# Performance work log

Measured on AMD Instinct MI355X. Metric: run time of the kernel, lower is better.

Reference implementation:

```python
import jax, jax.numpy as jnp
import numpy as np

VOCAB, EMBED, HIDDEN = 32000, 512, 1024
B, T = 2, 2048
LN_EPS = 1e-5


def setup_inputs() -> dict:
    key = jax.random.key(0)
    ks = jax.random.split(key, 12)

    def xavier(k, fan_in, fan_out):
        lim = float(np.sqrt(6.0 / (fan_in + fan_out)))
        return jax.random.uniform(k, (fan_in, fan_out), jnp.float32, -lim, lim)

    return {
        "tokens": jax.random.randint(ks[0], (B, T), 0, VOCAB),
        "E": xavier(ks[1], VOCAB, EMBED),                    # embedding table
        "Wc": xavier(ks[2], EMBED, HIDDEN),                  # fc_current (stored [in,out])
        "bc": jnp.full((HIDDEN,), 0.01, jnp.float32),
        "Wh": xavier(ks[3], EMBED, HIDDEN),                  # fc_context
        "bh": jnp.full((HIDDEN,), 0.01, jnp.float32),
        "Wm": xavier(ks[4], 2 * HIDDEN, HIDDEN),             # fc_merge
        "bm": jnp.full((HIDDEN,), 0.01, jnp.float32),
        "Wo": xavier(ks[5], HIDDEN, VOCAB),                  # fc_out
        "bo": jnp.full((VOCAB,), 0.01, jnp.float32),
        "ln_w": jnp.ones((HIDDEN,), jnp.float32),
        "ln_b": jnp.zeros((HIDDEN,), jnp.float32),
    }


def reference(tokens, E, Wc, bc, Wh, bh, Wm, bm, Wo, bo, ln_w, ln_b):
    emb = E[tokens]  # [B, T, D]
    # history mean at step t = mean(emb[:, :t]); at t==0 the module uses current embed
    csum = jnp.cumsum(emb, axis=1)
    counts = jnp.arange(1, T, dtype=emb.dtype)[None, :, None]
    hist_mean = jnp.concatenate([emb[:, :1], csum[:, :-1] / counts], axis=1)  # [B,T,D]

    cur_enc = jax.nn.relu(jnp.einsum("btd,dh->bth", emb, Wc) + bc)
    hist_enc = jax.nn.relu(jnp.einsum("btd,dh->bth", hist_mean, Wh) + bh)
    merged = jnp.concatenate([cur_enc, hist_enc], axis=-1)  # [B,T,2H]
    merged = jax.nn.relu(jnp.einsum("btk,kh->bth", merged, Wm) + bm)

    mu = jnp.mean(merged, axis=-1, keepdims=True)
    var = jnp.mean(jnp.square(merged - mu), axis=-1, keepdims=True)
    normed = (merged - mu) * jax.lax.rsqrt(var + LN_EPS) * ln_w + ln_b

    logits = (jnp.einsum("bth,hv->btv", normed, Wo) + bo) / 10.0  # [B,T,V]
    return logits
```

## Files before the change

### kernel.cpp

```cpp
#include <hip/hip_runtime.h>
#include <hip/hip_bf16.h>
#include <stdint.h>
#include <stdio.h>

#define T_SEQ  2048
#define BATCH  2
#define NROWS  4096
#define EMBED  512
#define HIDDEN 1024
#define VOCAB  32000
#define NCHUNK 32
#define CHLEN  64

typedef __bf16 bf16x8 __attribute__((ext_vector_type(8)));
typedef float  f32x4  __attribute__((ext_vector_type(4)));

__device__ __forceinline__ float b2f(unsigned short h) {
  union { unsigned int u; float f; } v; v.u = ((unsigned int)h) << 16; return v.f;
}
__device__ __forceinline__ unsigned short f2b(float f) {
  union { float f; unsigned int u; } v; v.f = f;
  unsigned int u = v.u;
  u += 0x7fffu + ((u >> 16) & 1u);
  return (unsigned short)(u >> 16);
}

__global__ void gather_kernel(const int* __restrict__ tokens,
                              const float* __restrict__ E,
                              unsigned short* __restrict__ emb) {
  const int row = blockIdx.x;
  const int tok = tokens[row];
  const float2 v = ((const float2*)(E + (size_t)tok * EMBED))[threadIdx.x];
  const uint32_t packed = (uint32_t)f2b(v.x) | ((uint32_t)f2b(v.y) << 16);
  ((uint32_t*)(emb + (size_t)row * EMBED))[threadIdx.x] = packed;
}

__global__ void scan_sum_kernel(const unsigned short* __restrict__ emb,
                                float* __restrict__ csum) {
  const int bc = blockIdx.x;
  const int d  = threadIdx.x;
  const unsigned short* e = emb + ((size_t)bc * CHLEN) * EMBED + d;
  float s = 0.f;
  #pragma unroll 8
  for (int i = 0; i < CHLEN; ++i) s += b2f(e[(size_t)i * EMBED]);
  csum[(size_t)bc * EMBED + d] = s;
}

__global__ void scan_excl_kernel(float* __restrict__ csum) {
  const int b = blockIdx.x;
  const int d = threadIdx.x;
  float run = 0.f;
  for (int c = 0; c < NCHUNK; ++c) {
    const size_t idx = ((size_t)b * NCHUNK + c) * EMBED + d;
    const float v = csum[idx];
    csum[idx] = run;
    run += v;
  }
}

__global__ void scan_emit_kernel(const unsigned short* __restrict__ emb,
                                 const float* __restrict__ csum,
                                 unsigned short* __restrict__ hist) {
  const int bc = blockIdx.x;
  const int c  = bc & (NCHUNK - 1);
  const int d  = threadIdx.x;
  const unsigned short* e = emb  + ((size_t)bc * CHLEN) * EMBED + d;
  unsigned short*       h = hist + ((size_t)bc * CHLEN) * EMBED + d;
  float sum = csum[(size_t)bc * EMBED + d];
  #pragma unroll 8
  for (int i = 0; i < CHLEN; ++i) {
    const int t = c * CHLEN + i;
    h[(size_t)i * EMBED] = (t == 0) ? e[0] : f2b(sum / (float)t);
    sum += b2f(e[(size_t)i * EMBED]);
  }
}

__global__ void transpose_cast_kernel(const float* __restrict__ in,
                                      unsigned short* __restrict__ out,
                                      int R, int C) {
  __shared__ float tile[32][33];
  const int tx = threadIdx.x & 31;
  const int ty = threadIdx.x >> 5;
  const int r0 = blockIdx.y * 32, c0 = blockIdx.x * 32;
  #pragma unroll
  for (int i = 0; i < 32; i += 8)
    tile[ty + i][tx] = in[(size_t)(r0 + ty + i) * C + (c0 + tx)];
  __syncthreads();
  #pragma unroll
  for (int i = 0; i < 32; i += 8)
    out[(size_t)(c0 + ty + i) * R + (r0 + tx)] = f2b(tile[tx][ty + i]);
}

__device__ __forceinline__ void async16(unsigned short* lds, const unsigned short* g) {
  __builtin_amdgcn_global_load_lds(
      (const __attribute__((address_space(1))) void*)g,
      (__attribute__((address_space(3))) void*)lds, 16, 0, 0);
}

#define BM 128
#define BN 128
#define BK 32

template<int MODE>
__global__ __launch_bounds__(256) void gemm_bt_kernel(
    const unsigned short* __restrict__ A,
    const unsigned short* __restrict__ BT,
    const float* __restrict__ bias,
    void* __restrict__ out, int M, int N, int K, int ldOut, int colOff,
    const unsigned short* __restrict__ A2,
    const unsigned short* __restrict__ BT2,
    const float* __restrict__ bias2, int colOff2) {
  __shared__ unsigned short As[BM * BK];
  __shared__ unsigned short Bs[BN * BK];

  const unsigned short* Ap = A;
  const unsigned short* Bp = BT;
  const float*          bp = bias;
  int                   co = colOff;
  if (blockIdx.z) { Ap = A2; Bp = BT2; bp = bias2; co = colOff2; }

  int wg = blockIdx.x;
  {
    const int nwg = gridDim.x;
    const int xcd = wg & 7, loc = wg >> 3;
    const int q = nwg >> 3, r = nwg & 7;
    wg = (xcd < r ? xcd * (q + 1) : r * (q + 1) + (xcd - r) * q) + loc;
  }
  const int nmb = M / BM;
  const int mb  = wg % nmb;
  const int nb  = wg / nmb;
  const int m0  = mb * BM;
  const int n0  = nb * BN;

  const int tid  = threadIdx.x;
  const int wave = tid >> 6;
  const int lane = tid & 63;
  const int wm = (wave & 1) * 64;
  const int wn = (wave >> 1) * 64;

  const int srow = (wave << 5) + (lane >> 2);
  const int scol = (lane & 3) << 3;
  const unsigned short* aSrc = Ap + (size_t)(m0 + srow) * K + scol;
  const unsigned short* bSrc = Bp + (size_t)(n0 + srow) * K + scol;
  unsigned short* aDst = As + (wave << 5) * BK;
  unsigned short* bDst = Bs + (wave << 5) * BK;

  f32x4 acc[4][4];
  #pragma unroll
  for (int i = 0; i < 4; ++i)
    #pragma unroll
    for (int j = 0; j < 4; ++j)
      acc[i][j] = (f32x4){0.f, 0.f, 0.f, 0.f};

  const int q = lane >> 4;
  const int r = lane & 15;

  for (int k0 = 0; k0 < K; k0 += BK) {
    __syncthreads();
    async16(aDst,           aSrc);
    async16(aDst + 16 * BK, aSrc + 16 * (size_t)K);
    async16(bDst,           bSrc);
    async16(bDst + 16 * BK, bSrc + 16 * (size_t)K);
    aSrc += BK; bSrc += BK;
    __syncthreads();

    bf16x8 af[4], bfr[4];
    #pragma unroll
    for (int mi = 0; mi < 4; ++mi)
      af[mi] = *(const bf16x8*)&As[(wm + mi * 16 + r) * BK + (q << 3)];
    #pragma unroll
    for (int ni = 0; ni < 4; ++ni)
      bfr[ni] = *(const bf16x8*)&Bs[(wn + ni * 16 + r) * BK + (q << 3)];
    #pragma unroll
    for (int mi = 0; mi < 4; ++mi)
      #pragma unroll
      for (int ni = 0; ni < 4; ++ni)
        acc[mi][ni] = __builtin_amdgcn_mfma_f32_16x16x32_bf16(
            af[mi], bfr[ni], acc[mi][ni], 0, 0, 0);
  }

  #pragma unroll
  for (int ni = 0; ni < 4; ++ni) {
    const int col = n0 + wn + ni * 16 + r;
    const float bv = bp[col];
    #pragma unroll
    for (int mi = 0; mi < 4; ++mi) {
      #pragma unroll
      for (int e = 0; e < 4; ++e) {
        const int row = m0 + wm + mi * 16 + (q << 2) + e;
        float v = acc[mi][ni][e] + bv;
        if (MODE == 0 || MODE == 1) v = fmaxf(v, 0.f);
        if (MODE == 2) v *= 0.1f;
        const size_t idx = (size_t)row * ldOut + co + col;
        if (MODE == 0) ((unsigned short*)out)[idx] = f2b(v);
        else           ((float*)out)[idx] = v;
      }
    }
  }
}


#define BAR() do {                            \
    asm volatile("" ::: "memory");            \
    __builtin_amdgcn_sched_barrier(0);        \
    __builtin_amdgcn_s_barrier();             \
    __builtin_amdgcn_sched_barrier(0);        \
    asm volatile("" ::: "memory");            \
  } while (0)

__global__ __launch_bounds__(512, 2) void gemm256_out_kernel(
    const unsigned short* __restrict__ A,
    const unsigned short* __restrict__ BT,
    const float* __restrict__ bias,
    float* __restrict__ out, int M, int N, int K, int ldOut) {
  __shared__ unsigned short lds[2][2][2][8192];

  int wg = blockIdx.x;
  {
    const int nwg = gridDim.x;
    const int xcd = wg & 7, loc = wg >> 3;
    const int q8 = nwg >> 3, r8 = nwg & 7;
    wg = (xcd < r8 ? xcd * (q8 + 1) : r8 * (q8 + 1) + (xcd - r8) * q8) + loc;
  }
  const int nmb = M >> 8;
  const int mb = wg % nmb, nb = wg / nmb;
  const int m0 = mb << 8, n0 = nb << 8;

  const int tid  = threadIdx.x;
  const int wave = tid >> 6, lane = tid & 63;
  const int wr = wave >> 2, wc = wave & 3;
  const int q = lane >> 4, r = lane & 15, rr = lane & 7;

  const int srow = (wave << 4) + (lane >> 3);
  const int scol = ((lane & 7) ^ (lane >> 3)) << 3;
  const unsigned short* aB = A  + (size_t)(m0 + srow) * K + scol;
  const unsigned short* bB = BT + (size_t)(n0 + srow) * K + scol;

  const int NTt = K >> 6;

  auto stage = [&](int matB, int h, int tb, int kt) {
    unsigned short* d = &lds[tb][matB][h][wave << 10];
    const unsigned short* s =
        (matB ? bB : aB) + (size_t)h * 128 * K + ((size_t)kt << 6);
    async16(d, s);
    async16(d + 512, s + ((size_t)K << 3));
  };

  auto ldA = [&](int tb, int mi, int ks) {
    return *(const bf16x8*)&lds[tb][0][wr]
        [(mi * 16 + r) * 64 + ((((ks << 2) | q) ^ rr) << 3)];
  };
  auto ldB = [&](int tb, int ni, int ks) {
    return *(const bf16x8*)&lds[tb][1][wc >> 1]
        [(((wc & 1) << 6) + ni * 16 + r) * 64 + ((((ks << 2) | q) ^ rr) << 3)];
  };

  f32x4 acc[8][4];
  #pragma unroll
  for (int i = 0; i < 8; ++i)
    #pragma unroll
    for (int j = 0; j < 4; ++j)
      acc[i][j] = (f32x4){0.f, 0.f, 0.f, 0.f};

  bf16x8 afr[8][2], bfr[2][2];

  stage(0, 0, 0, 0); stage(0, 1, 0, 0); stage(1, 0, 0, 0); stage(1, 1, 0, 0);
  if (NTt > 1) {
    stage(0, 0, 1, 1); stage(0, 1, 1, 1); stage(1, 0, 1, 1);
    asm volatile("s_waitcnt vmcnt(6)" ::: "memory");
  } else {
    asm volatile("s_waitcnt vmcnt(0)" ::: "memory");
  }
  BAR();

#define TILE(U, BU) do {                                                       \
    const int u_ = (U);                                                        \
                            \
    _Pragma("unroll")                                                          \
    for (int mi = 0; mi < 4; ++mi) {                                           \
      afr[mi][0] = ldA(BU, mi, 0); afr[mi][1] = ldA(BU, mi, 1);                \
    }                                                                          \
    _Pragma("unroll")                                                          \
    for (int nj = 0; nj < 2; ++nj) {                                           \
      bfr[nj][0] = ldB(BU, nj, 0); bfr[nj][1] = ldB(BU, nj, 1);                \
    }                                                                          \
    if (u_ + 1 < NTt) stage(1, 1, 1 - (BU), u_ + 1);                           \
    __builtin_amdgcn_s_setprio(1);                                             \
    _Pragma("unroll")                                                          \
    for (int mi = 0; mi < 4; ++mi)                                             \
      _Pragma("unroll")                                                        \
      for (int nj = 0; nj < 2; ++nj) {                                         \
        acc[mi][nj] = __builtin_amdgcn_mfma_f32_16x16x32_bf16(                 \
            afr[mi][0], bfr[nj][0], acc[mi][nj], 0, 0, 0);                     \
        acc[mi][nj] = __builtin_amdgcn_mfma_f32_16x16x32_bf16(                 \
            afr[mi][1], bfr[nj][1], acc[mi][nj], 0, 0, 0);                     \
      }                                                                        \
    __builtin_amdgcn_s_setprio(0);                                             \
    BAR();                                                                     \
                                 \
    _Pragma("unroll")                                                          \
    for (int mi = 4; mi < 8; ++mi) {                                           \
      afr[mi][0] = ldA(BU, mi, 0); afr[mi][1] = ldA(BU, mi, 1);                \
    }                                                                          \
    __builtin_amdgcn_s_setprio(1);                                             \
    _Pragma("unroll")                                                          \
    for (int mi = 4; mi < 8; ++mi)                                             \
      _Pragma("unroll")                                                        \
      for (int nj = 0; nj < 2; ++nj) {                                         \
        acc[mi][nj] = __builtin_amdgcn_mfma_f32_16x16x32_bf16(                 \
            afr[mi][0], bfr[nj][0], acc[mi][nj], 0, 0, 0);                     \
        acc[mi][nj] = __builtin_amdgcn_mfma_f32_16x16x32_bf16(                 \
            afr[mi][1], bfr[nj][1], acc[mi][nj], 0, 0, 0);                     \
      }                                                                        \
    __builtin_amdgcn_s_setprio(0);                                             \
    BAR();                                                                     \
                            \
    _Pragma("unroll")                                                          \
    for (int nj = 0; nj < 2; ++nj) {                                           \
      bfr[nj][0] = ldB(BU, 2 + nj, 0); bfr[nj][1] = ldB(BU, 2 + nj, 1);        \
    }                                                                          \
    if (u_ + 2 < NTt) stage(0, 0, BU, u_ + 2);                                 \
    __builtin_amdgcn_s_setprio(1);                                             \
    _Pragma("unroll")                                                          \
    for (int mi = 0; mi < 4; ++mi)                                             \
      _Pragma("unroll")                                                        \
      for (int nj = 0; nj < 2; ++nj) {                                         \
        acc[mi][2 + nj] = __builtin_amdgcn_mfma_f32_16x16x32_bf16(             \
            afr[mi][0], bfr[nj][0], acc[mi][2 + nj], 0, 0, 0);                 \
        acc[mi][2 + nj] = __builtin_amdgcn_mfma_f32_16x16x32_bf16(             \
            afr[mi][1], bfr[nj][1], acc[mi][2 + nj], 0, 0, 0);                 \
      }                                                                        \
    __builtin_amdgcn_s_setprio(0);                                             \
    BAR();                                                                     \
                   \
    if (u_ + 2 < NTt) { stage(0, 1, BU, u_ + 2); stage(1, 0, BU, u_ + 2); }    \
    __builtin_amdgcn_s_setprio(1);                                             \
    _Pragma("unroll")                                                          \
    for (int mi = 4; mi < 8; ++mi)                                             \
      _Pragma("unroll")                                                        \
      for (int nj = 0; nj < 2; ++nj) {                                         \
        acc[mi][2 + nj] = __builtin_amdgcn_mfma_f32_16x16x32_bf16(             \
            afr[mi][0], bfr[nj][0], acc[mi][2 + nj], 0, 0, 0);                 \
        acc[mi][2 + nj] = __builtin_amdgcn_mfma_f32_16x16x32_bf16(             \
            afr[mi][1], bfr[nj][1], acc[mi][2 + nj], 0, 0, 0);                 \
      }                                                                        \
    __builtin_amdgcn_s_setprio(0);                                             \
    if (u_ + 2 < NTt) asm volatile("s_waitcnt vmcnt(6)" ::: "memory");         \
    else              asm volatile("s_waitcnt vmcnt(0)" ::: "memory");         \
    BAR();                                                                     \
  } while (0)

  for (int u = 0; u < NTt; u += 2) {
    TILE(u, 0);
    TILE(u + 1, 1);
  }
#undef TILE

  #pragma unroll
  for (int ni = 0; ni < 4; ++ni) {
    const int col = n0 + (wc << 6) + ni * 16 + r;
    const float bv = bias[col];
    #pragma unroll
    for (int mi = 0; mi < 8; ++mi) {
      const int row = m0 + (wr << 7) + mi * 16 + (q << 2);
      #pragma unroll
      for (int e = 0; e < 4; ++e)
        out[(size_t)(row + e) * ldOut + col] = (acc[mi][ni][e] + bv) * 0.1f;
    }
  }
}

__global__ void ln_kernel(const float* __restrict__ merged,
                          const float* __restrict__ lnw,
                          const float* __restrict__ lnb,
                          unsigned short* __restrict__ normed) {
  const int row = blockIdx.x;
  const float4 v = ((const float4*)(merged + (size_t)row * HIDDEN))[threadIdx.x];
  float s  = v.x + v.y + v.z + v.w;
  float ss = v.x * v.x + v.y * v.y + v.z * v.z + v.w * v.w;
  #pragma unroll
  for (int off = 32; off > 0; off >>= 1) {
    s  += __shfl_down(s, off, 64);
    ss += __shfl_down(ss, off, 64);
  }
  __shared__ float red[8];
  const int wvi = threadIdx.x >> 6;
  if ((threadIdx.x & 63) == 0) { red[wvi] = s; red[4 + wvi] = ss; }
  __syncthreads();
  s  = red[0] + red[1] + red[2] + red[3];
  ss = red[4] + red[5] + red[6] + red[7];
  const float mu  = s * (1.0f / HIDDEN);
  const float var = ss * (1.0f / HIDDEN) - mu * mu;
  const float rs  = rsqrtf(var + 1e-5f);
  const float4 w4 = ((const float4*)lnw)[threadIdx.x];
  const float4 b4 = ((const float4*)lnb)[threadIdx.x];
  ushort4 o;
  o.x = f2b((v.x - mu) * rs * w4.x + b4.x);
  o.y = f2b((v.y - mu) * rs * w4.y + b4.y);
  o.z = f2b((v.z - mu) * rs * w4.z + b4.z);
  o.w = f2b((v.w - mu) * rs * w4.w + b4.w);
  ((ushort4*)(normed + (size_t)row * HIDDEN))[threadIdx.x] = o;
}

extern "C" void kernel_launch(void* const* d_in, const int* in_sizes, int n_in,
                              void* d_out, int out_size, void* d_ws, size_t ws_size,
                              hipStream_t stream) {
  const int*   tokens = (const int*)d_in[0];
  const float* E      = (const float*)d_in[1];
  const float* Wc     = (const float*)d_in[2];
  const float* bc     = (const float*)d_in[3];
  const float* Wh     = (const float*)d_in[4];
  const float* bh     = (const float*)d_in[5];
  const float* Wm     = (const float*)d_in[6];
  const float* bm     = (const float*)d_in[7];
  const float* Wo     = (const float*)d_in[8];
  const float* bo     = (const float*)d_in[9];
  const float* lnw    = (const float*)d_in[10];
  const float* lnb    = (const float*)d_in[11];

  char* p = (char*)d_ws;
  unsigned short* WcT  = (unsigned short*)p; p += (size_t)HIDDEN * EMBED * 2;
  unsigned short* WhT  = (unsigned short*)p; p += (size_t)HIDDEN * EMBED * 2;
  unsigned short* WmT  = (unsigned short*)p; p += (size_t)HIDDEN * (2 * HIDDEN) * 2;
  unsigned short* WoT  = (unsigned short*)p; p += (size_t)VOCAB * HIDDEN * 2;
  unsigned short* emb  = (unsigned short*)p; p += (size_t)NROWS * EMBED * 2;
  unsigned short* hist = (unsigned short*)p; p += (size_t)NROWS * EMBED * 2;
  unsigned short* cat  = (unsigned short*)p; p += (size_t)NROWS * (2 * HIDDEN) * 2;
  float*          mrg  = (float*)p;          p += (size_t)NROWS * HIDDEN * 4;
  unsigned short* nrm  = (unsigned short*)p; p += (size_t)NROWS * HIDDEN * 2;
  float*          csum = (float*)p;          p += (size_t)BATCH * NCHUNK * EMBED * 4;
  if ((size_t)(p - (char*)d_ws) > ws_size)
    fprintf(stderr, "WS TOO SMALL: need %zu have %zu\n", (size_t)(p - (char*)d_ws), ws_size);

  transpose_cast_kernel<<<dim3(HIDDEN / 32, EMBED / 32), 256, 0, stream>>>(Wc, WcT, EMBED, HIDDEN);
  transpose_cast_kernel<<<dim3(HIDDEN / 32, EMBED / 32), 256, 0, stream>>>(Wh, WhT, EMBED, HIDDEN);
  transpose_cast_kernel<<<dim3(HIDDEN / 32, (2 * HIDDEN) / 32), 256, 0, stream>>>(Wm, WmT, 2 * HIDDEN, HIDDEN);
  transpose_cast_kernel<<<dim3(VOCAB / 32, HIDDEN / 32), 256, 0, stream>>>(Wo, WoT, HIDDEN, VOCAB);

  gather_kernel<<<NROWS, 256, 0, stream>>>(tokens, E, emb);
  scan_sum_kernel <<<BATCH * NCHUNK, EMBED, 0, stream>>>(emb, csum);
  scan_excl_kernel<<<BATCH, EMBED, 0, stream>>>(csum);
  scan_emit_kernel<<<BATCH * NCHUNK, EMBED, 0, stream>>>(emb, csum, hist);

  const int nwgEnc = (NROWS / BM) * (HIDDEN / BN);

  gemm_bt_kernel<0><<<dim3(nwgEnc, 1, 2), 256, 0, stream>>>(
      emb, WcT, bc, cat, NROWS, HIDDEN, EMBED, 2 * HIDDEN, 0,
      hist, WhT, bh, HIDDEN);
  gemm_bt_kernel<1><<<dim3(nwgEnc, 1, 1), 256, 0, stream>>>(
      cat, WmT, bm, mrg, NROWS, HIDDEN, 2 * HIDDEN, HIDDEN, 0,
      nullptr, nullptr, nullptr, 0);
  ln_kernel<<<NROWS, 256, 0, stream>>>(mrg, lnw, lnb, nrm);

  const int nwgOut = (NROWS / 256) * (VOCAB / 256);
  gemm256_out_kernel<<<dim3(nwgOut), 512, 0, stream>>>(
      nrm, WoT, bo, (float*)d_out, NROWS, VOCAB, HIDDEN, VOCAB);
}
```

Baseline: 1.049 ms.

## Fuse weight transposes, fuse gather with chunk sum, stage output stores via LDS

Merges the four weight transpose-cast launches into a single kernel that uses 64x64 tiles with float4 loads and ushort4 stores. Fuses the embedding gather into the chunk-sum scan kernel, which removes one launch and one pass over the embeddings. The logits GEMM epilogue now stages each half of the output tile through swizzled LDS scratch so rows are written with coalesced 16-byte stores instead of scattered 4-byte ones. This adds two extra barriers per epilogue half. The fused gather runs on only 64 blocks, which may reduce parallelism for that stage.

```diff
diff --git a/kernel.cpp b/kernel.cpp
--- a/kernel.cpp
+++ b/kernel.cpp
@@ -25,24 +25,24 @@
   return (unsigned short)(u >> 16);
 }
 
-__global__ void gather_kernel(const int* __restrict__ tokens,
-                              const float* __restrict__ E,
-                              unsigned short* __restrict__ emb) {
-  const int row = blockIdx.x;
-  const int tok = tokens[row];
-  const float2 v = ((const float2*)(E + (size_t)tok * EMBED))[threadIdx.x];
-  const uint32_t packed = (uint32_t)f2b(v.x) | ((uint32_t)f2b(v.y) << 16);
-  ((uint32_t*)(emb + (size_t)row * EMBED))[threadIdx.x] = packed;
-}
-
-__global__ void scan_sum_kernel(const unsigned short* __restrict__ emb,
-                                float* __restrict__ csum) {
+__global__ void gather_sum_kernel(const int* __restrict__ tokens,
+                                  const float* __restrict__ E,
+                                  unsigned short* __restrict__ emb,
+                                  float* __restrict__ csum) {
   const int bc = blockIdx.x;
   const int d  = threadIdx.x;
-  const unsigned short* e = emb + ((size_t)bc * CHLEN) * EMBED + d;
+  __shared__ int tok[CHLEN];
+  if (d < CHLEN) tok[d] = tokens[bc * CHLEN + d];
+  __syncthreads();
   float s = 0.f;
-  #pragma unroll 8
-  for (int i = 0; i < CHLEN; ++i) s += b2f(e[(size_t)i * EMBED]);
+  unsigned short* eo = emb + ((size_t)bc * CHLEN) * EMBED + d;
+  #pragma unroll 4
+  for (int i = 0; i < CHLEN; ++i) {
+    const float v = E[(size_t)tok[i] * EMBED + d];
+    const unsigned short h = f2b(v);
+    eo[(size_t)i * EMBED] = h;
+    s += b2f(h);
+  }
   csum[(size_t)bc * EMBED + d] = s;
 }
 
@@ -75,20 +75,40 @@
   }
 }
 
-__global__ void transpose_cast_kernel(const float* __restrict__ in,
-                                      unsigned short* __restrict__ out,
-                                      int R, int C) {
-  __shared__ float tile[32][33];
-  const int tx = threadIdx.x & 31;
-  const int ty = threadIdx.x >> 5;
-  const int r0 = blockIdx.y * 32, c0 = blockIdx.x * 32;
-  #pragma unroll
-  for (int i = 0; i < 32; i += 8)
-    tile[ty + i][tx] = in[(size_t)(r0 + ty + i) * C + (c0 + tx)];
+__global__ __launch_bounds__(256) void transpose_all_kernel(
+    const float* __restrict__ Wc, const float* __restrict__ Wh,
+    const float* __restrict__ Wm, const float* __restrict__ Wo,
+    unsigned short* __restrict__ WcT, unsigned short* __restrict__ WhT,
+    unsigned short* __restrict__ WmT, unsigned short* __restrict__ WoT) {
+  const int id = blockIdx.x;
+  const float* in; unsigned short* out; int R, C, t;
+  if (id < 128)      { in = Wc; out = WcT; R = 512;  C = 1024;  t = id; }
+  else if (id < 256) { in = Wh; out = WhT; R = 512;  C = 1024;  t = id - 128; }
+  else if (id < 768) { in = Wm; out = WmT; R = 2048; C = 1024;  t = id - 256; }
+  else               { in = Wo; out = WoT; R = 1024; C = 32000; t = id - 768; }
+  const int tilesX = C >> 6;
+  const int r0 = (t / tilesX) << 6, c0 = (t % tilesX) << 6;
+
+  __shared__ float tile[64][65];
+  const int tid = threadIdx.x;
+  #pragma unroll
+  for (int p = 0; p < 4; ++p) {
+    const int u = tid + p * 256;
+    const int row = u >> 4, cq = (u & 15) << 2;
+    const float4 v = *(const float4*)&in[(size_t)(r0 + row) * C + c0 + cq];
+    tile[row][cq + 0] = v.x; tile[row][cq + 1] = v.y;
+    tile[row][cq + 2] = v.z; tile[row][cq + 3] = v.w;
+  }
   __syncthreads();
   #pragma unroll
-  for (int i = 0; i < 32; i += 8)
-    out[(size_t)(c0 + ty + i) * R + (r0 + tx)] = f2b(tile[tx][ty + i]);
+  for (int p = 0; p < 4; ++p) {
+    const int u = tid + p * 256;
+    const int oc = u >> 4, org = (u & 15) << 2;
+    ushort4 o;
+    o.x = f2b(tile[org + 0][oc]); o.y = f2b(tile[org + 1][oc]);
+    o.z = f2b(tile[org + 2][oc]); o.w = f2b(tile[org + 3][oc]);
+    *(ushort4*)&out[(size_t)(c0 + oc) * R + r0 + org] = o;
+  }
 }
 
 __device__ __forceinline__ void async16(unsigned short* lds, const unsigned short* g) {
@@ -188,9 +208,7 @@
       #pragma unroll
       for (int e = 0; e < 4; ++e) {
         const int row = m0 + wm + mi * 16 + (q << 2) + e;
-        float v = acc[mi][ni][e] + bv;
-        if (MODE == 0 || MODE == 1) v = fmaxf(v, 0.f);
-        if (MODE == 2) v *= 0.1f;
+        float v = fmaxf(acc[mi][ni][e] + bv, 0.f);
         const size_t idx = (size_t)row * ldOut + co + col;
         if (MODE == 0) ((unsigned short*)out)[idx] = f2b(v);
         else           ((float*)out)[idx] = v;
@@ -356,17 +374,34 @@
   }
 #undef TILE
 
-  #pragma unroll
-  for (int ni = 0; ni < 4; ++ni) {
-    const int col = n0 + (wc << 6) + ni * 16 + r;
-    const float bv = bias[col];
-    #pragma unroll
-    for (int mi = 0; mi < 8; ++mi) {
-      const int row = m0 + (wr << 7) + mi * 16 + (q << 2);
+  float* scratch = (float*)&lds[0][0][0][0];
+  #pragma unroll
+  for (int p = 0; p < 2; ++p) {
+    if (wr == p) {
       #pragma unroll
-      for (int e = 0; e < 4; ++e)
-        out[(size_t)(row + e) * ldOut + col] = (acc[mi][ni][e] + bv) * 0.1f;
+      for (int ni = 0; ni < 4; ++ni) {
+        const int col = (wc << 6) + ni * 16 + r;
+        const float bv = bias[n0 + col];
+        #pragma unroll
+        for (int mi = 0; mi < 8; ++mi) {
+          #pragma unroll
+          for (int e = 0; e < 4; ++e) {
+            const int row = mi * 16 + (q << 2) + e;
+            const int cs  = col ^ (((row >> 2) & 1) << 4);
+            scratch[row * 256 + cs] = (acc[mi][ni][e] + bv) * 0.1f;
+          }
+        }
+      }
     }
+    __syncthreads();
+    #pragma unroll
+    for (int rowi = 0; rowi < 16; ++rowi) {
+      const int row = (wave << 4) + rowi;
+      const int cb  = (lane << 2) ^ (((row >> 2) & 1) << 4);
+      const f32x4 v4 = *(const f32x4*)&scratch[row * 256 + cb];
+      *(f32x4*)&out[(size_t)(m0 + (p << 7) + row) * ldOut + n0 + (lane << 2)] = v4;
+    }
+    __syncthreads();
   }
 }
 
@@ -432,13 +467,9 @@
   if ((size_t)(p - (char*)d_ws) > ws_size)
     fprintf(stderr, "WS TOO SMALL: need %zu have %zu\n", (size_t)(p - (char*)d_ws), ws_size);
 
-  transpose_cast_kernel<<<dim3(HIDDEN / 32, EMBED / 32), 256, 0, stream>>>(Wc, WcT, EMBED, HIDDEN);
-  transpose_cast_kernel<<<dim3(HIDDEN / 32, EMBED / 32), 256, 0, stream>>>(Wh, WhT, EMBED, HIDDEN);
-  transpose_cast_kernel<<<dim3(HIDDEN / 32, (2 * HIDDEN) / 32), 256, 0, stream>>>(Wm, WmT, 2 * HIDDEN, HIDDEN);
-  transpose_cast_kernel<<<dim3(VOCAB / 32, HIDDEN / 32), 256, 0, stream>>>(Wo, WoT, HIDDEN, VOCAB);
-
-  gather_kernel<<<NROWS, 256, 0, stream>>>(tokens, E, emb);
-  scan_sum_kernel <<<BATCH * NCHUNK, EMBED, 0, stream>>>(emb, csum);
+  transpose_all_kernel<<<8768, 256, 0, stream>>>(Wc, Wh, Wm, Wo, WcT, WhT, WmT, WoT);
+
+  gather_sum_kernel<<<BATCH * NCHUNK, EMBED, 0, stream>>>(tokens, E, emb, csum);
   scan_excl_kernel<<<BATCH, EMBED, 0, stream>>>(csum);
   scan_emit_kernel<<<BATCH * NCHUNK, EMBED, 0, stream>>>(emb, csum, hist);
 
```

Result: faster. 986.2 us (-6.0%).
